# Optimization experiments

Hardware: AMD Instinct MI355X
Metric: run time of the kernel (lower is better)

The kernel has to match this reference:

```python
import jax, jax.numpy as jnp
import numpy as np

B, S, H, V, T = 512, 128, 1024, 4096, 32  # batch, enc len, hidden, output_size, max_length


def setup_inputs() -> dict:
    key = jax.random.key(0)
    ks = jax.random.split(key, 9)
    sc = 1.0 / np.sqrt(H).astype(np.float32)
    return {
        "encoder_outputs": jax.random.normal(ks[0], (B, S, H), jnp.float32),
        "sem_embs": jax.random.normal(ks[1], (B, S, H), jnp.float32),
        "embedding": jax.random.normal(ks[2], (V + 3, H), jnp.float32) * sc,
        "W_ih": jax.random.normal(ks[3], (3 * H, H), jnp.float32) * sc,
        "W_hh": jax.random.normal(ks[4], (3 * H, H), jnp.float32) * sc,
        "b_ih": jax.random.normal(ks[5], (3 * H,), jnp.float32) * sc,
        "b_hh": jax.random.normal(ks[6], (3 * H,), jnp.float32) * sc,
        "W_out": jax.random.normal(ks[7], (V, H), jnp.float32) * sc,
        "b_out": jax.random.normal(ks[8], (V,), jnp.float32) * sc,
    }


def gru_cell(x, h, W_ih, W_hh, b_ih, b_hh):
    # PyTorch GRU cell math: r,z,n gate order
    gi = x @ W_ih.T + b_ih
    gh = h @ W_hh.T + b_hh
    i_r, i_z, i_n = jnp.split(gi, 3, axis=-1)
    h_r, h_z, h_n = jnp.split(gh, 3, axis=-1)
    r = jax.nn.sigmoid(i_r + h_r)
    z = jax.nn.sigmoid(i_z + h_z)
    n = jnp.tanh(i_n + r * h_n)
    return (1.0 - z) * n + z * h


def reference(encoder_outputs, sem_embs, embedding, W_ih, W_hh, b_ih, b_hh, W_out, b_out):
    bs, _, hid = encoder_outputs.shape
    # init_batch: append fake EOS key/value embeddings (length mask is all-False -> no-op)
    fake_eos = jnp.broadcast_to(embedding[V][None, None, :], (bs, 1, hid))
    fake_eos_sem = jnp.broadcast_to(embedding[V + 1][None, None, :], (bs, 1, hid))
    keys = jnp.concatenate([encoder_outputs, fake_eos], axis=1)      # [B, S+1, H]
    values = jnp.concatenate([sem_embs, fake_eos_sem], axis=1)       # [B, S+1, H]
    scale = 1.0 / jnp.sqrt(jnp.asarray(hid, jnp.float32))

    def step(carry, _):
        tok, h = carry
        emb = embedding[tok]                                         # [B, H]
        h = gru_cell(emb, h, W_ih, W_hh, b_ih, b_hh)                 # [B, H]
        w = jax.nn.softmax(jnp.einsum('bh,bkh->bk', h, keys) * scale, axis=-1)  # [B, S+1]
        r = jnp.einsum('bk,bkh->bh', w, values)                      # [B, H]
        logits = (r + h) @ W_out.T + b_out                           # [B, V]
        logp = jax.nn.log_softmax(logits, axis=-1)
        x = jnp.argmax(logits, axis=-1)                              # eval-mode greedy decode
        lp = jnp.take_along_axis(logp, x[:, None], axis=-1)[:, 0]
        ent = -jnp.sum(jnp.exp(logp) * logp, axis=-1)
        return (x, h), (x, lp, ent, w)

    tok0 = jnp.full((bs,), V + 2, dtype=jnp.int32)  # SOS token = output_size + 2
    h0 = jnp.zeros((bs, hid), jnp.float32)
    _, (seq, lps, ents, ws) = jax.lax.scan(step, (tok0, h0), None, length=T)
    seq = jnp.moveaxis(seq, 0, 1)    # [B, T]
    lps = jnp.moveaxis(lps, 0, 1)
    ents = jnp.moveaxis(ents, 0, 1)
    ws = jnp.moveaxis(ws, 0, 1)      # [B, T, S+1]
    zf = jnp.zeros((bs, 1), jnp.float32)
    sequence = jnp.concatenate([seq, jnp.zeros((bs, 1), seq.dtype)], axis=-1)
    per_step_logits = jnp.concatenate([lps, zf], axis=-1)
    entropy = jnp.concatenate([ents, zf], axis=-1)
    return sequence, per_step_logits, entropy, ws
```

## Files before the change

### kernel.cpp

```cpp
#include <hip/hip_runtime.h>
#include <stdint.h>

#define HDIM 1024
#define NB   512
#define SEQ  128
#define VOUT 4096
#define TSTEPS 32
#define EROWS 4160

#define SEQ_OFF 0
#define LP_OFF  16896
#define ENT_OFF 33792
#define WS_OFF  50688

__global__ void init_kernel(float* __restrict__ h, int* __restrict__ tok,
                            float* __restrict__ out) {
  int idx = blockIdx.x * blockDim.x + threadIdx.x;
  h[idx] = 0.f;
  if (idx < NB) {
    tok[idx] = VOUT + 2;
    out[SEQ_OFF + idx * 33 + 32] = 0.f;
    out[LP_OFF  + idx * 33 + 32] = 0.f;
    out[ENT_OFF + idx * 33 + 32] = 0.f;
  }
}

__global__ __launch_bounds__(256) void gemm64_kernel(
    const float* __restrict__ A, const float* __restrict__ W,
    const float* __restrict__ bias, float* __restrict__ C,
    int N, int Mlim, int KLEN, int zstride) {
  __shared__ __align__(16) float Als[32][68];
  __shared__ __align__(16) float Bls[32][68];
  const int tid = threadIdx.x;
  const int tx = tid & 15, ty = tid >> 4;
  const int m0 = blockIdx.y * 64, n0 = blockIdx.x * 64;
  const int z = blockIdx.z;
  const int kbeg = z * KLEN;
  const int sr = tid >> 3;
  const int scol = (tid & 7) << 2;

  const int ca0 = sr ^ scol;
  const int ca1 = (sr + 32) ^ scol;

  const int ra = min(m0 + sr, Mlim - 1);
  const int rb = min(m0 + sr + 32, Mlim - 1);
  const float* a0 = A + (size_t)ra * HDIM + kbeg + scol;
  const float* a1 = A + (size_t)rb * HDIM + kbeg + scol;
  const float* w0 = W + (size_t)(n0 + sr) * HDIM + kbeg + scol;
  const float* w1 = W + (size_t)(n0 + sr + 32) * HDIM + kbeg + scol;

  float accT[4][4];
#pragma unroll
  for (int i = 0; i < 4; ++i)
#pragma unroll
    for (int j = 0; j < 4; ++j) accT[i][j] = 0.f;

  float4 av0 = *(const float4*)(a0);
  float4 av1 = *(const float4*)(a1);
  float4 wv0 = *(const float4*)(w0);
  float4 wv1 = *(const float4*)(w1);

  for (int k0 = 0; k0 < KLEN; k0 += 32) {
    __syncthreads();
    Als[scol + 0][ca0] = av0.x; Als[scol + 1][ca0] = av0.y;
    Als[scol + 2][ca0] = av0.z; Als[scol + 3][ca0] = av0.w;
    Als[scol + 0][ca1] = av1.x; Als[scol + 1][ca1] = av1.y;
    Als[scol + 2][ca1] = av1.z; Als[scol + 3][ca1] = av1.w;
    Bls[scol + 0][ca0] = wv0.x; Bls[scol + 1][ca0] = wv0.y;
    Bls[scol + 2][ca0] = wv0.z; Bls[scol + 3][ca0] = wv0.w;
    Bls[scol + 0][ca1] = wv1.x; Bls[scol + 1][ca1] = wv1.y;
    Bls[scol + 2][ca1] = wv1.z; Bls[scol + 3][ca1] = wv1.w;
    __syncthreads();

    {
      const int kn = min(k0 + 32, KLEN - 32);
      av0 = *(const float4*)(a0 + kn);
      av1 = *(const float4*)(a1 + kn);
      wv0 = *(const float4*)(w0 + kn);
      wv1 = *(const float4*)(w1 + kn);
    }

    float ac[4][4];
#pragma unroll
    for (int i = 0; i < 4; ++i)
#pragma unroll
      for (int j = 0; j < 4; ++j) ac[i][j] = 0.f;

#pragma unroll
    for (int kk = 0; kk < 32; ++kk) {
      const int sz = kk & 28;
      float4 a4 = *(const float4*)&Als[kk][(ty * 4) ^ sz];
      float4 b4 = *(const float4*)&Bls[kk][(tx * 4) ^ sz];
      float a_[4] = {a4.x, a4.y, a4.z, a4.w};
      float b_[4] = {b4.x, b4.y, b4.z, b4.w};
#pragma unroll
      for (int i = 0; i < 4; ++i)
#pragma unroll
        for (int j = 0; j < 4; ++j) ac[i][j] = fmaf(a_[i], b_[j], ac[i][j]);
    }
#pragma unroll
    for (int i = 0; i < 4; ++i)
#pragma unroll
      for (int j = 0; j < 4; ++j) accT[i][j] += ac[i][j];
  }

  float* Cz = C + (size_t)z * zstride;
  float b0 = 0.f, b1 = 0.f, b2 = 0.f, b3 = 0.f;
  if (z == 0) {
    b0 = bias[n0 + tx * 4 + 0];
    b1 = bias[n0 + tx * 4 + 1];
    b2 = bias[n0 + tx * 4 + 2];
    b3 = bias[n0 + tx * 4 + 3];
  }
#pragma unroll
  for (int i = 0; i < 4; ++i) {
    int m = m0 + ty * 4 + i;
    float4 o;
    o.x = accT[i][0] + b0;
    o.y = accT[i][1] + b1;
    o.z = accT[i][2] + b2;
    o.w = accT[i][3] + b3;
    *(float4*)&Cz[(size_t)m * N + n0 + tx * 4] = o;
  }
}

__global__ __launch_bounds__(256) void gate_kernel(
    const float* __restrict__ E2, const float* __restrict__ gh,
    const int* __restrict__ tok, float* __restrict__ h) {
  int idx = blockIdx.x * blockDim.x + threadIdx.x;
  int b = idx >> 8;
  int c = (idx & 255) << 2;
  const float* e = E2 + (size_t)tok[b] * (3 * HDIM) + c;
  const float* g0 = gh + (size_t)b * (3 * HDIM) + c;
  const float* g1 = g0 + (size_t)NB * 3 * HDIM;
  float4 ir = *(const float4*)(e);
  float4 iz = *(const float4*)(e + HDIM);
  float4 in_ = *(const float4*)(e + 2 * HDIM);
  float4 hra = *(const float4*)(g0);
  float4 hza = *(const float4*)(g0 + HDIM);
  float4 hna = *(const float4*)(g0 + 2 * HDIM);
  float4 hrb = *(const float4*)(g1);
  float4 hzb = *(const float4*)(g1 + HDIM);
  float4 hnb = *(const float4*)(g1 + 2 * HDIM);
  float4 hv = *(const float4*)&h[(size_t)b * HDIM + c];
  float4 o;
  {
    float r = 1.f / (1.f + expf(-(ir.x + hra.x + hrb.x)));
    float z = 1.f / (1.f + expf(-(iz.x + hza.x + hzb.x)));
    float n = tanhf(in_.x + r * (hna.x + hnb.x));
    o.x = (1.f - z) * n + z * hv.x;
  }
  {
    float r = 1.f / (1.f + expf(-(ir.y + hra.y + hrb.y)));
    float z = 1.f / (1.f + expf(-(iz.y + hza.y + hzb.y)));
    float n = tanhf(in_.y + r * (hna.y + hnb.y));
    o.y = (1.f - z) * n + z * hv.y;
  }
  {
    float r = 1.f / (1.f + expf(-(ir.z + hra.z + hrb.z)));
    float z = 1.f / (1.f + expf(-(iz.z + hza.z + hzb.z)));
    float n = tanhf(in_.z + r * (hna.z + hnb.z));
    o.z = (1.f - z) * n + z * hv.z;
  }
  {
    float r = 1.f / (1.f + expf(-(ir.w + hra.w + hrb.w)));
    float z = 1.f / (1.f + expf(-(iz.w + hza.w + hzb.w)));
    float n = tanhf(in_.w + r * (hna.w + hnb.w));
    o.w = (1.f - z) * n + z * hv.w;
  }
  *(float4*)&h[(size_t)b * HDIM + c] = o;
}

__global__ __launch_bounds__(1024) void attn_kernel(
    const float* __restrict__ h, const float* __restrict__ enc,
    const float* __restrict__ sem, const float* __restrict__ emb,
    float* __restrict__ x, float* __restrict__ out, int t) {
  const int b = blockIdx.x;
  const int tid = threadIdx.x;
  const int lane = tid & 63, wv = tid >> 6;
  __shared__ __align__(16) float hs[HDIM];
  __shared__ float uls[132];
  __shared__ float usums[16];
  __shared__ __align__(16) float accb[16][HDIM];

  hs[tid] = h[(size_t)b * HDIM + tid];
  __syncthreads();

  const int l4 = lane * 4;
  float4 hv0 = *(const float4*)&hs[l4];
  float4 hv1 = *(const float4*)&hs[l4 + 256];
  float4 hv2 = *(const float4*)&hs[l4 + 512];
  float4 hv3 = *(const float4*)&hs[l4 + 768];

  float4 acc0 = {0, 0, 0, 0}, acc1 = {0, 0, 0, 0};
  float4 acc2 = {0, 0, 0, 0}, acc3 = {0, 0, 0, 0};
  float usum = 0.f;

  for (int k = wv; k < SEQ + 1; k += 16) {
    const float* kr;
    const float* vr;
    if (k < SEQ) {
      kr = enc + ((size_t)b * SEQ + k) * HDIM;
      vr = sem + ((size_t)b * SEQ + k) * HDIM;
    } else {
      kr = emb + (size_t)VOUT * HDIM;
      vr = emb + (size_t)(VOUT + 1) * HDIM;
    }
    float4 e0 = *(const float4*)(kr + l4);
    float4 e1 = *(const float4*)(kr + l4 + 256);
    float4 e2 = *(const float4*)(kr + l4 + 512);
    float4 e3 = *(const float4*)(kr + l4 + 768);
    float4 v0 = *(const float4*)(vr + l4);
    float4 v1 = *(const float4*)(vr + l4 + 256);
    float4 v2 = *(const float4*)(vr + l4 + 512);
    float4 v3 = *(const float4*)(vr + l4 + 768);

    float p = 0.f;
    p = fmaf(e0.x, hv0.x, p); p = fmaf(e0.y, hv0.y, p);
    p = fmaf(e0.z, hv0.z, p); p = fmaf(e0.w, hv0.w, p);
    p = fmaf(e1.x, hv1.x, p); p = fmaf(e1.y, hv1.y, p);
    p = fmaf(e1.z, hv1.z, p); p = fmaf(e1.w, hv1.w, p);
    p = fmaf(e2.x, hv2.x, p); p = fmaf(e2.y, hv2.y, p);
    p = fmaf(e2.z, hv2.z, p); p = fmaf(e2.w, hv2.w, p);
    p = fmaf(e3.x, hv3.x, p); p = fmaf(e3.y, hv3.y, p);
    p = fmaf(e3.z, hv3.z, p); p = fmaf(e3.w, hv3.w, p);
#pragma unroll
    for (int off = 32; off; off >>= 1) p += __shfl_xor(p, off);

    float u = expf(p * 0.03125f);
    usum += u;
    if (lane == 0) uls[k] = u;

    acc0.x = fmaf(u, v0.x, acc0.x); acc0.y = fmaf(u, v0.y, acc0.y);
    acc0.z = fmaf(u, v0.z, acc0.z); acc0.w = fmaf(u, v0.w, acc0.w);
    acc1.x = fmaf(u, v1.x, acc1.x); acc1.y = fmaf(u, v1.y, acc1.y);
    acc1.z = fmaf(u, v1.z, acc1.z); acc1.w = fmaf(u, v1.w, acc1.w);
    acc2.x = fmaf(u, v2.x, acc2.x); acc2.y = fmaf(u, v2.y, acc2.y);
    acc2.z = fmaf(u, v2.z, acc2.z); acc2.w = fmaf(u, v2.w, acc2.w);
    acc3.x = fmaf(u, v3.x, acc3.x); acc3.y = fmaf(u, v3.y, acc3.y);
    acc3.z = fmaf(u, v3.z, acc3.z); acc3.w = fmaf(u, v3.w, acc3.w);
  }

  if (lane == 0) usums[wv] = usum;
  *(float4*)&accb[wv][l4] = acc0;
  *(float4*)&accb[wv][l4 + 256] = acc1;
  *(float4*)&accb[wv][l4 + 512] = acc2;
  *(float4*)&accb[wv][l4 + 768] = acc3;
  __syncthreads();

  float U = 0.f;
#pragma unroll
  for (int w = 0; w < 16; ++w) U += usums[w];
  float rinv = 1.f / U;

  float sum = 0.f;
#pragma unroll
  for (int w = 0; w < 16; ++w) sum += accb[w][tid];
  x[(size_t)b * HDIM + tid] = sum * rinv + hs[tid];

  if (tid < SEQ + 1)
    out[WS_OFF + ((size_t)b * TSTEPS + t) * (SEQ + 1) + tid] = uls[tid] * rinv;
}

__global__ __launch_bounds__(256) void finalize_kernel(
    const float* __restrict__ logits, float* __restrict__ out,
    int* __restrict__ tok, int t) {
  const int b = blockIdx.x, tid = threadIdx.x;
  const int lane = tid & 63, wv = tid >> 6;
  const float* lrow = logits + (size_t)b * VOUT;
  float m = -3.4e38f; int mi = 0;
  float s = 0.f, ts = 0.f;
#pragma unroll
  for (int it = 0; it < 4; ++it) {
    int j = (tid << 2) + (it << 10);
    float4 v = *(const float4*)&lrow[j];
    float e;
    e = expf(v.x); s += e; ts = fmaf(e, v.x, ts); if (v.x > m) { m = v.x; mi = j; }
    e = expf(v.y); s += e; ts = fmaf(e, v.y, ts); if (v.y > m) { m = v.y; mi = j + 1; }
    e = expf(v.z); s += e; ts = fmaf(e, v.z, ts); if (v.z > m) { m = v.z; mi = j + 2; }
    e = expf(v.w); s += e; ts = fmaf(e, v.w, ts); if (v.w > m) { m = v.w; mi = j + 3; }
  }
#pragma unroll
  for (int off = 32; off; off >>= 1) {
    float om = __shfl_xor(m, off);
    int oi = __shfl_xor(mi, off);
    s += __shfl_xor(s, off);
    ts += __shfl_xor(ts, off);
    if (om > m || (om == m && oi < mi)) { m = om; mi = oi; }
  }
  __shared__ float smx[4], ssm[4], sts[4];
  __shared__ int smi[4];
  if (lane == 0) { smx[wv] = m; smi[wv] = mi; ssm[wv] = s; sts[wv] = ts; }
  __syncthreads();
  if (tid == 0) {
#pragma unroll
    for (int w = 1; w < 4; ++w) {
      s += ssm[w]; ts += sts[w];
      if (smx[w] > m || (smx[w] == m && smi[w] < mi)) { m = smx[w]; mi = smi[w]; }
    }
    float lse = logf(s);
    float lp = m - lse;
    float ent = lse - ts / s;
    out[SEQ_OFF + (size_t)b * 33 + t] = (float)mi;
    out[LP_OFF  + (size_t)b * 33 + t] = lp;
    out[ENT_OFF + (size_t)b * 33 + t] = ent;
    tok[b] = mi;
  }
}

extern "C" void kernel_launch(void* const* d_in, const int* in_sizes, int n_in,
                              void* d_out, int out_size, void* d_ws, size_t ws_size,
                              hipStream_t stream) {
  const float* enc   = (const float*)d_in[0];
  const float* sem   = (const float*)d_in[1];
  const float* emb   = (const float*)d_in[2];
  const float* W_ih  = (const float*)d_in[3];
  const float* W_hh  = (const float*)d_in[4];
  const float* b_ih  = (const float*)d_in[5];
  const float* b_hh  = (const float*)d_in[6];
  const float* W_out = (const float*)d_in[7];
  const float* b_out = (const float*)d_in[8];
  float* out = (float*)d_out;

  float* h      = (float*)d_ws;
  float* x      = h + (size_t)NB * HDIM;
  float* gh     = x + (size_t)NB * HDIM;
  float* logits = gh + (size_t)2 * NB * 3 * HDIM;
  float* E2     = logits + (size_t)NB * VOUT;
  int*   tok    = (int*)(E2 + (size_t)EROWS * 3 * HDIM);

  init_kernel<<<2048, 256, 0, stream>>>(h, tok, out);
  gemm64_kernel<<<dim3(48, 65, 1), 256, 0, stream>>>(emb, W_ih, b_ih, E2,
                                                     3 * HDIM, VOUT + 3, HDIM, 0);

  for (int t = 0; t < TSTEPS; ++t) {
    gemm64_kernel<<<dim3(48, 8, 2), 256, 0, stream>>>(h, W_hh, b_hh, gh,
                                                      3 * HDIM, NB, HDIM / 2,
                                                      NB * 3 * HDIM);
    gate_kernel<<<512, 256, 0, stream>>>(E2, gh, tok, h);
    attn_kernel<<<512, 1024, 0, stream>>>(h, enc, sem, emb, x, out, t);
    gemm64_kernel<<<dim3(64, 8, 1), 256, 0, stream>>>(x, W_out, b_out, logits,
                                                      VOUT, NB, HDIM, 0);
    finalize_kernel<<<512, 256, 0, stream>>>(logits, out, tok, t);
  }
}
```

Baseline: 7.827 ms.

## Co-schedule attention with next-step W_hh GEMM and fuse argmax with GRU gate

Restructures the per-step schedule. The recurrent h@W_hh GEMM for step t+1 now runs in the same launch as step t's attention, with extra blocks handling 128x64 split-K tiles, since both read only the current h. The argmax/log-softmax finalize is fused with the GRU gate update, so the next token's embedding projection is gathered directly. This cuts launches from five to three per step and lets the bandwidth-bound attention overlap the compute-bound GEMM, at the cost of a prologue launch, smaller attention blocks (512 threads) and a hand-written GEMM path.

```diff
diff --git a/kernel.cpp b/kernel.cpp
--- a/kernel.cpp
+++ b/kernel.cpp
@@ -171,100 +171,197 @@
   *(float4*)&h[(size_t)b * HDIM + c] = o;
 }
 
-__global__ __launch_bounds__(1024) void attn_kernel(
+#define SMEM_BYTES 37440
+__global__ __launch_bounds__(512) void attn_gh_kernel(
     const float* __restrict__ h, const float* __restrict__ enc,
     const float* __restrict__ sem, const float* __restrict__ emb,
-    float* __restrict__ x, float* __restrict__ out, int t) {
-  const int b = blockIdx.x;
+    float* __restrict__ x, float* __restrict__ out, int t,
+    const float* __restrict__ W_hh, const float* __restrict__ b_hh,
+    float* __restrict__ gh, int nattn) {
+  __shared__ __align__(16) char smem[SMEM_BYTES];
   const int tid = threadIdx.x;
-  const int lane = tid & 63, wv = tid >> 6;
-  __shared__ __align__(16) float hs[HDIM];
-  __shared__ float uls[132];
-  __shared__ float usums[16];
-  __shared__ __align__(16) float accb[16][HDIM];
-
-  hs[tid] = h[(size_t)b * HDIM + tid];
-  __syncthreads();
-
-  const int l4 = lane * 4;
-  float4 hv0 = *(const float4*)&hs[l4];
-  float4 hv1 = *(const float4*)&hs[l4 + 256];
-  float4 hv2 = *(const float4*)&hs[l4 + 512];
-  float4 hv3 = *(const float4*)&hs[l4 + 768];
-
-  float4 acc0 = {0, 0, 0, 0}, acc1 = {0, 0, 0, 0};
-  float4 acc2 = {0, 0, 0, 0}, acc3 = {0, 0, 0, 0};
-  float usum = 0.f;
-
-  for (int k = wv; k < SEQ + 1; k += 16) {
-    const float* kr;
-    const float* vr;
-    if (k < SEQ) {
-      kr = enc + ((size_t)b * SEQ + k) * HDIM;
-      vr = sem + ((size_t)b * SEQ + k) * HDIM;
-    } else {
-      kr = emb + (size_t)VOUT * HDIM;
-      vr = emb + (size_t)(VOUT + 1) * HDIM;
-    }
-    float4 e0 = *(const float4*)(kr + l4);
-    float4 e1 = *(const float4*)(kr + l4 + 256);
-    float4 e2 = *(const float4*)(kr + l4 + 512);
-    float4 e3 = *(const float4*)(kr + l4 + 768);
-    float4 v0 = *(const float4*)(vr + l4);
-    float4 v1 = *(const float4*)(vr + l4 + 256);
-    float4 v2 = *(const float4*)(vr + l4 + 512);
-    float4 v3 = *(const float4*)(vr + l4 + 768);
-
-    float p = 0.f;
-    p = fmaf(e0.x, hv0.x, p); p = fmaf(e0.y, hv0.y, p);
-    p = fmaf(e0.z, hv0.z, p); p = fmaf(e0.w, hv0.w, p);
-    p = fmaf(e1.x, hv1.x, p); p = fmaf(e1.y, hv1.y, p);
-    p = fmaf(e1.z, hv1.z, p); p = fmaf(e1.w, hv1.w, p);
-    p = fmaf(e2.x, hv2.x, p); p = fmaf(e2.y, hv2.y, p);
-    p = fmaf(e2.z, hv2.z, p); p = fmaf(e2.w, hv2.w, p);
-    p = fmaf(e3.x, hv3.x, p); p = fmaf(e3.y, hv3.y, p);
-    p = fmaf(e3.z, hv3.z, p); p = fmaf(e3.w, hv3.w, p);
-#pragma unroll
-    for (int off = 32; off; off >>= 1) p += __shfl_xor(p, off);
-
-    float u = expf(p * 0.03125f);
-    usum += u;
-    if (lane == 0) uls[k] = u;
-
-    acc0.x = fmaf(u, v0.x, acc0.x); acc0.y = fmaf(u, v0.y, acc0.y);
-    acc0.z = fmaf(u, v0.z, acc0.z); acc0.w = fmaf(u, v0.w, acc0.w);
-    acc1.x = fmaf(u, v1.x, acc1.x); acc1.y = fmaf(u, v1.y, acc1.y);
-    acc1.z = fmaf(u, v1.z, acc1.z); acc1.w = fmaf(u, v1.w, acc1.w);
-    acc2.x = fmaf(u, v2.x, acc2.x); acc2.y = fmaf(u, v2.y, acc2.y);
-    acc2.z = fmaf(u, v2.z, acc2.z); acc2.w = fmaf(u, v2.w, acc2.w);
-    acc3.x = fmaf(u, v3.x, acc3.x); acc3.y = fmaf(u, v3.y, acc3.y);
-    acc3.z = fmaf(u, v3.z, acc3.z); acc3.w = fmaf(u, v3.w, acc3.w);
-  }
-
-  if (lane == 0) usums[wv] = usum;
-  *(float4*)&accb[wv][l4] = acc0;
-  *(float4*)&accb[wv][l4 + 256] = acc1;
-  *(float4*)&accb[wv][l4 + 512] = acc2;
-  *(float4*)&accb[wv][l4 + 768] = acc3;
-  __syncthreads();
-
-  float U = 0.f;
-#pragma unroll
-  for (int w = 0; w < 16; ++w) U += usums[w];
-  float rinv = 1.f / U;
-
-  float sum = 0.f;
-#pragma unroll
-  for (int w = 0; w < 16; ++w) sum += accb[w][tid];
-  x[(size_t)b * HDIM + tid] = sum * rinv + hs[tid];
-
-  if (tid < SEQ + 1)
-    out[WS_OFF + ((size_t)b * TSTEPS + t) * (SEQ + 1) + tid] = uls[tid] * rinv;
-}
-
-__global__ __launch_bounds__(256) void finalize_kernel(
-    const float* __restrict__ logits, float* __restrict__ out,
-    int* __restrict__ tok, int t) {
+  if ((int)blockIdx.x < nattn) {
+    float* hs = reinterpret_cast<float*>(smem);
+    float (*accb)[HDIM] = reinterpret_cast<float (*)[HDIM]>(smem + 4096);
+    float* uls = reinterpret_cast<float*>(smem + 36864);
+    float* usums = reinterpret_cast<float*>(smem + 37392);
+    const int b = blockIdx.x;
+    const int lane = tid & 63, wv = tid >> 6;
+
+    *(float2*)&hs[tid * 2] = *(const float2*)&h[(size_t)b * HDIM + tid * 2];
+    __syncthreads();
+
+    const int l4 = lane * 4;
+    float4 hv0 = *(const float4*)&hs[l4];
+    float4 hv1 = *(const float4*)&hs[l4 + 256];
+    float4 hv2 = *(const float4*)&hs[l4 + 512];
+    float4 hv3 = *(const float4*)&hs[l4 + 768];
+
+    float4 acc0 = {0, 0, 0, 0}, acc1 = {0, 0, 0, 0};
+    float4 acc2 = {0, 0, 0, 0}, acc3 = {0, 0, 0, 0};
+    float usum = 0.f;
+
+    for (int k = wv; k < SEQ + 1; k += 8) {
+      const float* kr;
+      const float* vr;
+      if (k < SEQ) {
+        kr = enc + ((size_t)b * SEQ + k) * HDIM;
+        vr = sem + ((size_t)b * SEQ + k) * HDIM;
+      } else {
+        kr = emb + (size_t)VOUT * HDIM;
+        vr = emb + (size_t)(VOUT + 1) * HDIM;
+      }
+      float4 e0 = *(const float4*)(kr + l4);
+      float4 e1 = *(const float4*)(kr + l4 + 256);
+      float4 e2 = *(const float4*)(kr + l4 + 512);
+      float4 e3 = *(const float4*)(kr + l4 + 768);
+      float4 v0 = *(const float4*)(vr + l4);
+      float4 v1 = *(const float4*)(vr + l4 + 256);
+      float4 v2 = *(const float4*)(vr + l4 + 512);
+      float4 v3 = *(const float4*)(vr + l4 + 768);
+
+      float p = 0.f;
+      p = fmaf(e0.x, hv0.x, p); p = fmaf(e0.y, hv0.y, p);
+      p = fmaf(e0.z, hv0.z, p); p = fmaf(e0.w, hv0.w, p);
+      p = fmaf(e1.x, hv1.x, p); p = fmaf(e1.y, hv1.y, p);
+      p = fmaf(e1.z, hv1.z, p); p = fmaf(e1.w, hv1.w, p);
+      p = fmaf(e2.x, hv2.x, p); p = fmaf(e2.y, hv2.y, p);
+      p = fmaf(e2.z, hv2.z, p); p = fmaf(e2.w, hv2.w, p);
+      p = fmaf(e3.x, hv3.x, p); p = fmaf(e3.y, hv3.y, p);
+      p = fmaf(e3.z, hv3.z, p); p = fmaf(e3.w, hv3.w, p);
+#pragma unroll
+      for (int off = 32; off; off >>= 1) p += __shfl_xor(p, off);
+
+      float u = expf(p * 0.03125f);
+      usum += u;
+      if (lane == 0) uls[k] = u;
+
+      acc0.x = fmaf(u, v0.x, acc0.x); acc0.y = fmaf(u, v0.y, acc0.y);
+      acc0.z = fmaf(u, v0.z, acc0.z); acc0.w = fmaf(u, v0.w, acc0.w);
+      acc1.x = fmaf(u, v1.x, acc1.x); acc1.y = fmaf(u, v1.y, acc1.y);
+      acc1.z = fmaf(u, v1.z, acc1.z); acc1.w = fmaf(u, v1.w, acc1.w);
+      acc2.x = fmaf(u, v2.x, acc2.x); acc2.y = fmaf(u, v2.y, acc2.y);
+      acc2.z = fmaf(u, v2.z, acc2.z); acc2.w = fmaf(u, v2.w, acc2.w);
+      acc3.x = fmaf(u, v3.x, acc3.x); acc3.y = fmaf(u, v3.y, acc3.y);
+      acc3.z = fmaf(u, v3.z, acc3.z); acc3.w = fmaf(u, v3.w, acc3.w);
+    }
+
+    if (lane == 0) usums[wv] = usum;
+    *(float4*)&accb[wv][l4] = acc0;
+    *(float4*)&accb[wv][l4 + 256] = acc1;
+    *(float4*)&accb[wv][l4 + 512] = acc2;
+    *(float4*)&accb[wv][l4 + 768] = acc3;
+    __syncthreads();
+
+    float U = 0.f;
+#pragma unroll
+    for (int w = 0; w < 8; ++w) U += usums[w];
+    float rinv = 1.f / U;
+
+#pragma unroll
+    for (int dd = 0; dd < 2; ++dd) {
+      int d = tid + dd * 512;
+      float sum = 0.f;
+#pragma unroll
+      for (int w = 0; w < 8; ++w) sum += accb[w][d];
+      x[(size_t)b * HDIM + d] = sum * rinv + hs[d];
+    }
+
+    if (tid < SEQ + 1)
+      out[WS_OFF + ((size_t)b * TSTEPS + t) * (SEQ + 1) + tid] = uls[tid] * rinv;
+  } else {
+    float (*Als)[132] = reinterpret_cast<float (*)[132]>(smem);
+    float (*Bls)[68] = reinterpret_cast<float (*)[68]>(smem + 16896);
+    int gb = blockIdx.x - nattn;
+    const int z = gb / 192; gb -= z * 192;
+    const int by = gb / 48, bx = gb - by * 48;
+    const int m0 = by * 128, n0 = bx * 64;
+    const int kbeg = z * 512;
+    const int tx = tid & 15, ty = tid >> 4;
+    const int sr = tid >> 3;
+    const int scol = (tid & 7) << 2;
+    const int ca = sr ^ scol;
+
+    const float* a0 = h + (size_t)(m0 + sr) * HDIM + kbeg + scol;
+    const float* a1 = h + (size_t)(m0 + sr + 64) * HDIM + kbeg + scol;
+    const float* w0 = W_hh + (size_t)(n0 + sr) * HDIM + kbeg + scol;
+
+    float accT[4][4];
+#pragma unroll
+    for (int i = 0; i < 4; ++i)
+#pragma unroll
+      for (int j = 0; j < 4; ++j) accT[i][j] = 0.f;
+
+    float4 av0 = *(const float4*)(a0);
+    float4 av1 = *(const float4*)(a1);
+    float4 wv0 = *(const float4*)(w0);
+
+    for (int k0 = 0; k0 < 512; k0 += 32) {
+      __syncthreads();
+      Als[scol + 0][ca] = av0.x; Als[scol + 1][ca] = av0.y;
+      Als[scol + 2][ca] = av0.z; Als[scol + 3][ca] = av0.w;
+      Als[scol + 0][ca + 64] = av1.x; Als[scol + 1][ca + 64] = av1.y;
+      Als[scol + 2][ca + 64] = av1.z; Als[scol + 3][ca + 64] = av1.w;
+      Bls[scol + 0][ca] = wv0.x; Bls[scol + 1][ca] = wv0.y;
+      Bls[scol + 2][ca] = wv0.z; Bls[scol + 3][ca] = wv0.w;
+      __syncthreads();
+
+      {
+        const int kn = min(k0 + 32, 512 - 32);
+        av0 = *(const float4*)(a0 + kn);
+        av1 = *(const float4*)(a1 + kn);
+        wv0 = *(const float4*)(w0 + kn);
+      }
+
+      float ac[4][4];
+#pragma unroll
+      for (int i = 0; i < 4; ++i)
+#pragma unroll
+        for (int j = 0; j < 4; ++j) ac[i][j] = 0.f;
+
+#pragma unroll
+      for (int kk = 0; kk < 32; ++kk) {
+        const int sz = kk & 28;
+        float4 a4 = *(const float4*)&Als[kk][(ty * 4) ^ sz];
+        float4 b4 = *(const float4*)&Bls[kk][(tx * 4) ^ sz];
+        float a_[4] = {a4.x, a4.y, a4.z, a4.w};
+        float b_[4] = {b4.x, b4.y, b4.z, b4.w};
+#pragma unroll
+        for (int i = 0; i < 4; ++i)
+#pragma unroll
+          for (int j = 0; j < 4; ++j) ac[i][j] = fmaf(a_[i], b_[j], ac[i][j]);
+      }
+#pragma unroll
+      for (int i = 0; i < 4; ++i)
+#pragma unroll
+        for (int j = 0; j < 4; ++j) accT[i][j] += ac[i][j];
+    }
+
+    float* Cz = gh + (size_t)z * (NB * 3 * HDIM);
+    float b0 = 0.f, b1 = 0.f, b2 = 0.f, b3 = 0.f;
+    if (z == 0) {
+      b0 = b_hh[n0 + tx * 4 + 0];
+      b1 = b_hh[n0 + tx * 4 + 1];
+      b2 = b_hh[n0 + tx * 4 + 2];
+      b3 = b_hh[n0 + tx * 4 + 3];
+    }
+#pragma unroll
+    for (int i = 0; i < 4; ++i) {
+      int m = m0 + ty * 4 + i;
+      float4 o;
+      o.x = accT[i][0] + b0;
+      o.y = accT[i][1] + b1;
+      o.z = accT[i][2] + b2;
+      o.w = accT[i][3] + b3;
+      *(float4*)&Cz[(size_t)m * (3 * HDIM) + n0 + tx * 4] = o;
+    }
+  }
+}
+
+__global__ __launch_bounds__(256) void finalgate_kernel(
+    const float* __restrict__ logits, float* __restrict__ out, int t,
+    const float* __restrict__ E2, const float* __restrict__ gh,
+    float* __restrict__ h) {
   const int b = blockIdx.x, tid = threadIdx.x;
   const int lane = tid & 63, wv = tid >> 6;
   const float* lrow = logits + (size_t)b * VOUT;
@@ -290,6 +387,7 @@
   }
   __shared__ float smx[4], ssm[4], sts[4];
   __shared__ int smi[4];
+  __shared__ int mib;
   if (lane == 0) { smx[wv] = m; smi[wv] = mi; ssm[wv] = s; sts[wv] = ts; }
   __syncthreads();
   if (tid == 0) {
@@ -304,8 +402,50 @@
     out[SEQ_OFF + (size_t)b * 33 + t] = (float)mi;
     out[LP_OFF  + (size_t)b * 33 + t] = lp;
     out[ENT_OFF + (size_t)b * 33 + t] = ent;
-    tok[b] = mi;
-  }
+    mib = mi;
+  }
+  __syncthreads();
+
+  const int c = tid << 2;
+  const float* e = E2 + (size_t)mib * (3 * HDIM) + c;
+  const float* g0 = gh + (size_t)b * (3 * HDIM) + c;
+  const float* g1 = g0 + (size_t)NB * 3 * HDIM;
+  float4 ir = *(const float4*)(e);
+  float4 iz = *(const float4*)(e + HDIM);
+  float4 in_ = *(const float4*)(e + 2 * HDIM);
+  float4 hra = *(const float4*)(g0);
+  float4 hza = *(const float4*)(g0 + HDIM);
+  float4 hna = *(const float4*)(g0 + 2 * HDIM);
+  float4 hrb = *(const float4*)(g1);
+  float4 hzb = *(const float4*)(g1 + HDIM);
+  float4 hnb = *(const float4*)(g1 + 2 * HDIM);
+  float4 hv = *(const float4*)&h[(size_t)b * HDIM + c];
+  float4 o;
+  {
+    float r = 1.f / (1.f + expf(-(ir.x + hra.x + hrb.x)));
+    float z = 1.f / (1.f + expf(-(iz.x + hza.x + hzb.x)));
+    float n = tanhf(in_.x + r * (hna.x + hnb.x));
+    o.x = (1.f - z) * n + z * hv.x;
+  }
+  {
+    float r = 1.f / (1.f + expf(-(ir.y + hra.y + hrb.y)));
+    float z = 1.f / (1.f + expf(-(iz.y + hza.y + hzb.y)));
+    float n = tanhf(in_.y + r * (hna.y + hnb.y));
+    o.y = (1.f - z) * n + z * hv.y;
+  }
+  {
+    float r = 1.f / (1.f + expf(-(ir.z + hra.z + hrb.z)));
+    float z = 1.f / (1.f + expf(-(iz.z + hza.z + hzb.z)));
+    float n = tanhf(in_.z + r * (hna.z + hnb.z));
+    o.z = (1.f - z) * n + z * hv.z;
+  }
+  {
+    float r = 1.f / (1.f + expf(-(ir.w + hra.w + hrb.w)));
+    float z = 1.f / (1.f + expf(-(iz.w + hza.w + hzb.w)));
+    float n = tanhf(in_.w + r * (hna.w + hnb.w));
+    o.w = (1.f - z) * n + z * hv.w;
+  }
+  *(float4*)&h[(size_t)b * HDIM + c] = o;
 }
 
 extern "C" void kernel_launch(void* const* d_in, const int* in_sizes, int n_in,
@@ -332,15 +472,15 @@
   init_kernel<<<2048, 256, 0, stream>>>(h, tok, out);
   gemm64_kernel<<<dim3(48, 65, 1), 256, 0, stream>>>(emb, W_ih, b_ih, E2,
                                                      3 * HDIM, VOUT + 3, HDIM, 0);
+  attn_gh_kernel<<<384, 512, 0, stream>>>(h, enc, sem, emb, x, out, 0,
+                                          W_hh, b_hh, gh, 0);
+  gate_kernel<<<512, 256, 0, stream>>>(E2, gh, tok, h);
 
   for (int t = 0; t < TSTEPS; ++t) {
-    gemm64_kernel<<<dim3(48, 8, 2), 256, 0, stream>>>(h, W_hh, b_hh, gh,
-                                                      3 * HDIM, NB, HDIM / 2,
-                                                      NB * 3 * HDIM);
-    gate_kernel<<<512, 256, 0, stream>>>(E2, gh, tok, h);
-    attn_kernel<<<512, 1024, 0, stream>>>(h, enc, sem, emb, x, out, t);
+    attn_gh_kernel<<<896, 512, 0, stream>>>(h, enc, sem, emb, x, out, t,
+                                            W_hh, b_hh, gh, 512);
     gemm64_kernel<<<dim3(64, 8, 1), 256, 0, stream>>>(x, W_out, b_out, logits,
                                                       VOUT, NB, HDIM, 0);
-    finalize_kernel<<<512, 256, 0, stream>>>(logits, out, tok, t);
-  }
-}
+    finalgate_kernel<<<512, 256, 0, stream>>>(logits, out, t, E2, gh, h);
+  }
+}
```

Result: faster. 7.520 ms, median of 2 (-3.9%).
